# Kernel tuning notes

Hardware: AMD Instinct MI355X
Metric: run time of the kernel (lower is better)

## Reference

```python
import jax, jax.numpy as jnp
import numpy as np
from jax import lax


def setup_inputs() -> dict:
    key = jax.random.key(0)
    k1, k2 = jax.random.split(key)
    N, D_IN, D_MODEL, ORDER_K = 8192, 1024, 1024, 8
    scale = 1.0 / np.sqrt(D_IN)
    x = jax.random.normal(k1, (N, D_IN), dtype=jnp.float32)
    weights = jax.random.normal(k2, (ORDER_K + 1, D_IN, D_MODEL), dtype=jnp.float32) * scale
    return {"x": x, "weights": weights}


def reference(x, weights):
    # x: [N, d_in]; weights: [K+1, d_in, d_model]
    x32 = x.astype(jnp.float32)
    t0 = jnp.ones_like(x32)                      # T_0(x) = 1
    out = t0 @ weights[0] + x32 @ weights[1]     # T_0 W_0 + T_1 W_1

    def step(carry, w_k):
        prev2, prev1, acc = carry
        tk = 2.0 * x32 * prev1 - prev2           # Chebyshev recurrence T_k
        acc = acc + tk @ w_k
        return (prev1, tk, acc), None

    (_, _, out), _ = lax.scan(step, (t0, x32, out), weights[2:])
    return out
```

## Files before the change

kernel.cpp:

```cpp
#include <hip/hip_runtime.h>
#include <hip/hip_bf16.h>
#include <stdint.h>

typedef float  f32x4  __attribute__((ext_vector_type(4)));
typedef short  s16x8  __attribute__((ext_vector_type(8)));

#define GLOAD_LDS16(g, l)                                                          \
  __builtin_amdgcn_global_load_lds(                                               \
      (const __attribute__((address_space(1))) unsigned int*)(g),                 \
      (__attribute__((address_space(3))) unsigned int*)(l), 16, 0, 0)

#define WAITVM_(N) asm volatile("s_waitcnt vmcnt(" #N ")" ::: "memory")
#define WAITVM(N) WAITVM_(N)
#define WAITLGKM0 asm volatile("s_waitcnt lgkmcnt(0)" ::: "memory")

static __device__ __forceinline__ unsigned short f2bf(float f) {
  union { __hip_bfloat16 b; unsigned short s; } cv;
  cv.b = __float2bfloat16(f);
  return cv.s;
}

static __device__ __forceinline__ int swz_e(int r) { return ((r & 3) ^ ((r >> 2) & 1)); }
static __device__ __forceinline__ int swz_byte(int r, int c) {
  return r * 64 + (((c ^ swz_e(r)) & 3) << 4);
}

__global__ __launch_bounds__(256) void agen(const float* __restrict__ x,
                                            short* __restrict__ amat) {
  const int g = blockIdx.x * 256 + threadIdx.x;
  const int row = g >> 7;
  const int d0 = (g & 127) << 3;
  const float* xp = x + (size_t)row * 1024 + d0;
  f32x4 a = *(const f32x4*)xp, b = *(const f32x4*)(xp + 4);
  float p1[8], p2[8], x2[8];
  #pragma unroll
  for (int i = 0; i < 8; ++i) {
    float v = (i < 4) ? a[i] : b[i - 4];
    p1[i] = v; p2[i] = 1.f; x2[i] = v + v;
  }
  short* dst = amat + (size_t)row * 8192 + d0;
  #pragma unroll
  for (int k = 1; k <= 8; ++k) {
    union { unsigned short u[8]; s16x8 v; } o;
    #pragma unroll
    for (int i = 0; i < 8; ++i) o.u[i] = f2bf(p1[i]);
    *(s16x8*)(dst + (size_t)(k - 1) * 1024) = o.v;
    if (k < 8) {
      #pragma unroll
      for (int i = 0; i < 8; ++i) {
        float c = fmaf(x2[i], p1[i], -p2[i]);
        p2[i] = p1[i]; p1[i] = c;
      }
    }
  }
}

__global__ __launch_bounds__(256) void transpose_w2(const float* __restrict__ w,
                                                    short* __restrict__ wt) {
  __shared__ unsigned int ldsT[64 * 33];
  const int t = threadIdx.x;
  const int bid = blockIdx.x;
  const int kk = bid >> 8;
  const int db = (bid >> 4) & 15;
  const int cb = bid & 15;
  const int d0 = db * 64, c0 = cb * 64;
  const float* src = w + (size_t)(kk + 1) * 1048576 + (size_t)d0 * 1024 + c0;
  #pragma unroll
  for (int p = 0; p < 4; ++p) {
    int dl = p * 16 + (t >> 4);
    int c4 = (t & 15) * 4;
    f32x4 f = *(const f32x4*)(src + (size_t)dl * 1024 + c4);
    unsigned lo = (unsigned)f2bf(f.x) | ((unsigned)f2bf(f.y) << 16);
    unsigned hi = (unsigned)f2bf(f.z) | ((unsigned)f2bf(f.w) << 16);
    ldsT[dl * 33 + (t & 15) * 2]     = lo;
    ldsT[dl * 33 + (t & 15) * 2 + 1] = hi;
  }
  __syncthreads();
  const int col = t >> 2;
  const int dc  = t & 3;
  union { unsigned short u[8]; s16x8 v; } o0, o1;
  #pragma unroll
  for (int j = 0; j < 16; ++j) {
    int dl = dc * 16 + j;
    unsigned word = ldsT[dl * 33 + (col >> 1)];
    unsigned short e = (col & 1) ? (unsigned short)(word >> 16) : (unsigned short)(word & 0xffffu);
    if (j < 8) o0.u[j] = e; else o1.u[j - 8] = e;
  }
  short* dst = wt + (size_t)(c0 + col) * 8192 + (size_t)kk * 1024 + d0 + dc * 16;
  *(s16x8*)dst       = o0.v;
  *(s16x8*)(dst + 8) = o1.v;
}

__global__ __launch_bounds__(256) void transpose_w(const float* __restrict__ w,
                                                   short* __restrict__ wt) {
  __shared__ unsigned int ldsT[64 * 33];
  const int t = threadIdx.x;
  const int bid = blockIdx.x;
  const int kb = bid >> 8;
  const int db = (bid >> 4) & 15;
  const int cb = bid & 15;
  const int d0 = db * 64, c0 = cb * 64;
  const float* src = w + (size_t)(kb + 1) * 1048576 + (size_t)d0 * 1024 + c0;
  #pragma unroll
  for (int p = 0; p < 4; ++p) {
    int dl = p * 16 + (t >> 4);
    int c4 = (t & 15) * 4;
    f32x4 f = *(const f32x4*)(src + (size_t)dl * 1024 + c4);
    unsigned lo = (unsigned)f2bf(f.x) | ((unsigned)f2bf(f.y) << 16);
    unsigned hi = (unsigned)f2bf(f.z) | ((unsigned)f2bf(f.w) << 16);
    ldsT[dl * 33 + (t & 15) * 2]     = lo;
    ldsT[dl * 33 + (t & 15) * 2 + 1] = hi;
  }
  __syncthreads();
  const int col = t >> 2;
  const int dc  = t & 3;
  union { unsigned short u[8]; s16x8 v; } o0, o1;
  #pragma unroll
  for (int j = 0; j < 16; ++j) {
    int dl = dc * 16 + j;
    unsigned word = ldsT[dl * 33 + (col >> 1)];
    unsigned short e = (col & 1) ? (unsigned short)(word >> 16) : (unsigned short)(word & 0xffffu);
    if (j < 8) o0.u[j] = e; else o1.u[j - 8] = e;
  }
  short* dst = wt + ((size_t)(kb * 1024 + c0 + col) * 1024 + d0 + dc * 16);
  *(s16x8*)dst       = o0.v;
  *(s16x8*)(dst + 8) = o1.v;
}

__global__ __launch_bounds__(256) void bias_k(const float* __restrict__ w,
                                              float* __restrict__ b) {
  __shared__ float red[256];
  const int t = threadIdx.x;
  const int col = blockIdx.x * 64 + (t & 63);
  const int seg = t >> 6;
  float s = 0.f;
  const float* p = w + (size_t)(seg * 256) * 1024 + col;
  for (int d = 0; d < 256; ++d) s += p[(size_t)d * 1024];
  red[t] = s;
  __syncthreads();
  if (t < 64) b[col] = red[t] + red[t + 64] + red[t + 128] + red[t + 192];
}

__global__ __launch_bounds__(256) void init_out(const float* __restrict__ bias,
                                                float* __restrict__ out, int has_bias) {
  const size_t i = (size_t)blockIdx.x * 256 + threadIdx.x;
  const int c = (int)((i * 4) & 1023);
  f32x4 v = has_bias ? *(const f32x4*)(bias + c) : (f32x4){0.f, 0.f, 0.f, 0.f};
  *(f32x4*)(out + i * 4) = v;
}

__global__ __launch_bounds__(512, 2) void gemm8(
    const short* __restrict__ amat, const short* __restrict__ wt2,
    float* __restrict__ out) {
  __shared__ __attribute__((aligned(16))) char lds[131072];

  const int tid = threadIdx.x, lane = tid & 63, wid = tid >> 6;
  const int bid = blockIdx.x;
  const int xcd = bid & 7, mb = bid >> 3;
  const int nb = xcd >> 1, kb = xcd & 1;
  const int rowbase = mb * 256, colbase = nb * 256;
  const int wr = wid >> 2, wc = wid & 3;
  const int la = lane & 15, lg = lane >> 4;
  const int ela = (la & 3) ^ ((la >> 2) & 1);

  int aoff[4], boff[4];
  #pragma unroll
  for (int mm = 0; mm < 4; ++mm)
    aoff[mm] = ((wr * 128 + mm * 16 + la) << 6) + ((lg ^ ela) << 4);
  #pragma unroll
  for (int n = 0; n < 4; ++n)
    boff[n] = 65536 + ((wc * 64 + n * 16 + la) << 6) + ((lg ^ ela) << 4);

  const int rr   = lane >> 2;
  const int goff = ((lane & 3) ^ ((rr & 3) ^ ((rr >> 2) & 1))) * 8;
  const int r0 = wid * 32 + rr, r1 = r0 + 16;
  const size_t kk0 = (size_t)kb * 4096;
  const short* asrc0 = amat + (size_t)(rowbase + r0) * 8192 + kk0 + goff;
  const short* asrc1 = amat + (size_t)(rowbase + r1) * 8192 + kk0 + goff;
  const short* bsrc0 = wt2 + (size_t)(colbase + r0) * 8192 + kk0 + goff;
  const short* bsrc1 = wt2 + (size_t)(colbase + r1) * 8192 + kk0 + goff;
  const int adst0 = wid * 2048, adst1 = adst0 + 1024;

  f32x4 acc[8][4];
  #pragma unroll
  for (int m = 0; m < 8; ++m)
    #pragma unroll
    for (int n = 0; n < 4; ++n) acc[m][n] = (f32x4){0.f, 0.f, 0.f, 0.f};

#define STAGE_A(T, SOFF)                                                           \
  { GLOAD_LDS16(asrc0 + (T) * 32, lds + (SOFF) + adst0);                           \
    GLOAD_LDS16(asrc1 + (T) * 32, lds + (SOFF) + adst1); }
#define STAGE_B(T, SOFF)                                                           \
  { GLOAD_LDS16(bsrc0 + (T) * 32, lds + 65536 + (SOFF) + adst0);                   \
    GLOAD_LDS16(bsrc1 + (T) * 32, lds + 65536 + (SOFF) + adst1); }

  STAGE_A(0, 0);     STAGE_B(0, 0);
  STAGE_A(1, 16384); STAGE_B(1, 16384);
  WAITVM(4);
  __builtin_amdgcn_sched_barrier(0);
  __builtin_amdgcn_s_barrier();
  __builtin_amdgcn_sched_barrier(0);

  #pragma unroll 1
  for (int t = 0; t < 128; ++t) {
    const int soff = (t & 3) << 14;
    const int s2   = ((t + 2) & 3) << 14;
    s16x8 bf[4], af[4];

    #pragma unroll
    for (int n = 0; n < 4; ++n) bf[n] = *(const s16x8*)(lds + soff + boff[n]);
    #pragma unroll
    for (int mm = 0; mm < 4; ++mm) af[mm] = *(const s16x8*)(lds + soff + aoff[mm]);
    if (t + 2 < 128) STAGE_A(t + 2, s2);
    __builtin_amdgcn_s_barrier();
    WAITLGKM0;
    __builtin_amdgcn_sched_barrier(0);
    __builtin_amdgcn_s_setprio(1);
    #pragma unroll
    for (int n = 0; n < 4; ++n)
      #pragma unroll
      for (int mm = 0; mm < 4; ++mm)
        acc[mm][n] = __builtin_amdgcn_mfma_f32_16x16x32_bf16(af[mm], bf[n], acc[mm][n], 0, 0, 0);
    __builtin_amdgcn_s_setprio(0);
    __builtin_amdgcn_sched_barrier(0);
    __builtin_amdgcn_s_barrier();
    __builtin_amdgcn_sched_barrier(0);

    #pragma unroll
    for (int mm = 0; mm < 4; ++mm) af[mm] = *(const s16x8*)(lds + soff + 4096 + aoff[mm]);
    if (t + 2 < 128) STAGE_B(t + 2, s2);
    __builtin_amdgcn_s_barrier();
    WAITLGKM0;
    __builtin_amdgcn_sched_barrier(0);
    __builtin_amdgcn_s_setprio(1);
    #pragma unroll
    for (int n = 0; n < 4; ++n)
      #pragma unroll
      for (int mm = 0; mm < 4; ++mm)
        acc[4 + mm][n] = __builtin_amdgcn_mfma_f32_16x16x32_bf16(af[mm], bf[n], acc[4 + mm][n], 0, 0, 0);
    __builtin_amdgcn_s_setprio(0);
    if (t < 126) { WAITVM(4); } else { WAITVM(0); }
    __builtin_amdgcn_sched_barrier(0);
    __builtin_amdgcn_s_barrier();
    __builtin_amdgcn_sched_barrier(0);
  }
#undef STAGE_A
#undef STAGE_B

  #pragma unroll
  for (int m = 0; m < 8; ++m) {
    const int r0o = rowbase + wr * 128 + m * 16 + lg * 4;
    #pragma unroll
    for (int n = 0; n < 4; ++n) {
      const int c = colbase + wc * 64 + n * 16 + la;
      #pragma unroll
      for (int j = 0; j < 4; ++j)
        unsafeAtomicAdd(&out[(size_t)(r0o + j) * 1024 + c], acc[m][n][j]);
    }
  }
}

template <bool USE_WS>
__global__ __launch_bounds__(256, 2) void cheb_gemm(
    const float* __restrict__ x, const float* __restrict__ w,
    const short* __restrict__ wt, float* __restrict__ out) {
  __shared__ short Asm[2][4096];
  __shared__ short Bsm[3][8192];

  const int tid = threadIdx.x, lane = tid & 63, wid = tid >> 6;
  const int bid = blockIdx.x;
  const int xcd = bid & 7;
  const int mb  = bid >> 3;
  const int nb  = xcd >> 1, kb = xcd & 1;
  const int rowbase = mb * 128, colbase = nb * 256;
  const int kbase = kb * 512;
  const int wr = wid >> 1, wc = wid & 1;
  const int la = lane & 15, lg = lane >> 4;
  const int e_la = (la & 3) ^ ((la >> 2) & 1);
  const int abase = (wr * 64 + la) * 64 + ((lg ^ e_la) << 4);
  const int bbase = (wc * 128 + la) * 64 + ((lg ^ e_la) << 4);

  const int arow = tid & 127, h = tid >> 7;
  const int aw0 = swz_byte(arow, 2 * h), aw1 = swz_byte(arow, 2 * h + 1);
  const float* xrow = x + (size_t)(rowbase + arow) * 1024 + kbase + h * 16;

  float p1[16], p2[16];
  unsigned x2h[8];
  f32x4 xq[4];
  f32x4 acc[4][8];
  #pragma unroll
  for (int m = 0; m < 4; ++m)
    #pragma unroll
    for (int n = 0; n < 8; ++n) acc[m][n] = (f32x4){0.f, 0.f, 0.f, 0.f};

  if constexpr (USE_WS) {
    const int bcol0  = wid * 64 + (lane >> 2);
    const int goff   = ((lane & 3) ^ swz_e(lane >> 2)) * 8;
    const short* gptr = wt + (size_t)(colbase + bcol0) * 1024 + kbase + goff;

#define ISSUE_AT(PTR, WOFF)                                                        \
    { _Pragma("unroll")                                                            \
      for (int j_ = 0; j_ < 4; ++j_)                                               \
        GLOAD_LDS16((PTR) + j_ * 16384,                                            \
                    (char*)&Bsm[0][0] + (WOFF) + (wid * 4 + j_) * 1024); }

    #pragma unroll
    for (int q = 0; q < 4; ++q) xq[q] = *(const f32x4*)(xrow + q * 4);
    ISSUE_AT(gptr, 0);          gptr += 1048576;
    ISSUE_AT(gptr, 16384);      gptr += 1048576;
    {
      union { unsigned short u[8]; s16x8 v; } o0, o1;
      #pragma unroll
      for (int i = 0; i < 16; ++i) { p1[i] = xq[i >> 2][i & 3]; p2[i] = 1.f; }
      #pragma unroll
      for (int i = 0; i < 8; ++i) {
        union { unsigned u; _Float16 f[2]; } t2;
        t2.f[0] = (_Float16)(p1[2 * i] + p1[2 * i]);
        t2.f[1] = (_Float16)(p1[2 * i + 1] + p1[2 * i + 1]);
        x2h[i] = t2.u;
        o0.u[i] = f2bf(p1[i]); o1.u[i] = f2bf(p1[i + 8]);
      }
      *(s16x8*)((char*)&Asm[0][0] + aw0) = o0.v;
      *(s16x8*)((char*)&Asm[0][0] + aw1) = o1.v;
    }
    WAITLGKM0;
    WAITVM(4);
    __builtin_amdgcn_sched_barrier(0);
    __builtin_amdgcn_s_barrier();
    __builtin_amdgcn_sched_barrier(0);

    int wroff = 32768, rdoff = 0, ard = 0;

    #pragma unroll 1
    for (int t = 0; t < 128; ++t) {
      if ((t & 7) == 2 && t < 120) {
        const float* xs = xrow + ((t >> 3) + 1) * 32;
        #pragma unroll
        for (int q = 0; q < 4; ++q) xq[q] = *(const f32x4*)(xs + q * 4);
      }
      if (t + 2 < 128) {
        ISSUE_AT(gptr, wroff);
        gptr += ((t & 7) == 5) ? (32 - 7 * 1048576) : 1048576;
        wroff = (wroff == 32768) ? 0 : wroff + 16384;
      }
      if (t + 1 < 128) {
        const int rn = (t + 1) & 7;
        union { unsigned short u[8]; s16x8 v; } o0, o1;
        if (rn == 0) {
          #pragma unroll
          for (int i = 0; i < 16; ++i) { p1[i] = xq[i >> 2][i & 3]; p2[i] = 1.f; }
          #pragma unroll
          for (int i = 0; i < 8; ++i) {
            union { unsigned u; _Float16 f[2]; } t2;
            t2.f[0] = (_Float16)(p1[2 * i] + p1[2 * i]);
            t2.f[1] = (_Float16)(p1[2 * i + 1] + p1[2 * i + 1]);
            x2h[i] = t2.u;
            o0.u[i] = f2bf(p1[i]); o1.u[i] = f2bf(p1[i + 8]);
          }
        } else {
          #pragma unroll
          for (int i = 0; i < 16; ++i) {
            union { unsigned u; _Float16 f[2]; } t2; t2.u = x2h[i >> 1];
            float cur = fmaf((float)t2.f[i & 1], p1[i], -p2[i]);
            p2[i] = p1[i]; p1[i] = cur;
            unsigned short e = f2bf(cur);
            if (i < 8) o0.u[i] = e; else o1.u[i - 8] = e;
          }
        }
        *(s16x8*)((char*)&Asm[0][0] + (ard ^ 8192) + aw0) = o0.v;
        *(s16x8*)((char*)&Asm[0][0] + (ard ^ 8192) + aw1) = o1.v;
      }
      s16x8 af[4];
      #pragma unroll
      for (int m = 0; m < 4; ++m)
        af[m] = *(const s16x8*)((char*)&Asm[0][0] + ard + abase + m * 1024);
      #pragma unroll
      for (int n = 0; n < 8; ++n) {
        s16x8 bfr = *(const s16x8*)((char*)&Bsm[0][0] + rdoff + bbase + n * 1024);
        #pragma unroll
        for (int m = 0; m < 4; ++m)
          acc[m][n] = __builtin_amdgcn_mfma_f32_16x16x32_bf16(af[m], bfr, acc[m][n], 0, 0, 0);
      }
      WAITLGKM0;
      if (t < 126) { WAITVM(4); } else { WAITVM(0); }
      __builtin_amdgcn_sched_barrier(0);
      __builtin_amdgcn_s_barrier();
      __builtin_amdgcn_sched_barrier(0);
      rdoff = (rdoff == 32768) ? 0 : rdoff + 16384;
      ard ^= 8192;
    }
#undef ISSUE_AT
  } else {
    #pragma unroll 1
    for (int s = 0; s < 144; ++s) {
      const int r = s % 9, st = s / 9;
      const int d0 = kbase + st * 32;
      __syncthreads();
      { const int dd = tid & 31, cg = tid >> 5;
        const float* ws_ = w + (size_t)r * 1048576 + (size_t)(d0 + dd) * 1024 + colbase + cg * 4;
        #pragma unroll
        for (int p_ = 0; p_ < 8; ++p_) {
          f32x4 f_ = *(const f32x4*)(ws_ + p_ * 32);
          #pragma unroll
          for (int jj = 0; jj < 4; ++jj) {
            int col = cg * 4 + p_ * 32 + jj;
            int byt = col * 64 + ((dd & 7) << 1) + ((((dd >> 3) ^ swz_e(col)) & 3) << 4);
            *(unsigned short*)((char*)&Bsm[0][0] + byt) = f2bf(f_[jj]);
          } } }
      union { unsigned short u[8]; s16x8 v; } o0, o1;
      if (r == 0) {
        #pragma unroll
        for (int q = 0; q < 4; ++q) xq[q] = *(const f32x4*)(xrow + st * 32 + q * 4);
        #pragma unroll
        for (int i = 0; i < 16; ++i) { p1[i] = xq[i >> 2][i & 3]; p2[i] = 1.f; }
        #pragma unroll
        for (int i = 0; i < 8; ++i) {
          union { unsigned u; _Float16 f[2]; } t2;
          t2.f[0] = (_Float16)(p1[2 * i] + p1[2 * i]);
          t2.f[1] = (_Float16)(p1[2 * i + 1] + p1[2 * i + 1]);
          x2h[i] = t2.u;
          o0.u[i] = 0x3f80; o1.u[i] = 0x3f80;
        }
      } else if (r == 1) {
        #pragma unroll
        for (int i = 0; i < 8; ++i) { o0.u[i] = f2bf(p1[i]); o1.u[i] = f2bf(p1[i + 8]); }
      } else {
        #pragma unroll
        for (int i = 0; i < 16; ++i) {
          union { unsigned u; _Float16 f[2]; } t2; t2.u = x2h[i >> 1];
          float cur = fmaf((float)t2.f[i & 1], p1[i], -p2[i]);
          p2[i] = p1[i]; p1[i] = cur;
          if (i < 8) o0.u[i] = f2bf(cur); else o1.u[i - 8] = f2bf(cur);
        }
      }
      *(s16x8*)((char*)&Asm[0][0] + aw0) = o0.v;
      *(s16x8*)((char*)&Asm[0][0] + aw1) = o1.v;
      __syncthreads();
      s16x8 af[4];
      #pragma unroll
      for (int m = 0; m < 4; ++m)
        af[m] = *(const s16x8*)((char*)&Asm[0][0] + abase + m * 1024);
      #pragma unroll
      for (int n = 0; n < 8; ++n) {
        s16x8 bfr = *(const s16x8*)((char*)&Bsm[0][0] + bbase + n * 1024);
        #pragma unroll
        for (int m = 0; m < 4; ++m)
          acc[m][n] = __builtin_amdgcn_mfma_f32_16x16x32_bf16(af[m], bfr, acc[m][n], 0, 0, 0);
      }
    }
  }

  #pragma unroll
  for (int m = 0; m < 4; ++m) {
    const int r0 = rowbase + wr * 64 + m * 16 + lg * 4;
    #pragma unroll
    for (int n = 0; n < 8; ++n) {
      const int c = colbase + wc * 128 + n * 16 + la;
      #pragma unroll
      for (int j = 0; j < 4; ++j)
        unsafeAtomicAdd(&out[(size_t)(r0 + j) * 1024 + c], acc[m][n][j]);
    }
  }
}

extern "C" void kernel_launch(void* const* d_in, const int* in_sizes, int n_in,
                              void* d_out, int out_size, void* d_ws, size_t ws_size,
                              hipStream_t stream) {
  const float* x = (const float*)d_in[0];
  const float* w = (const float*)d_in[1];
  float* out = (float*)d_out;

  const size_t AMAT_BYTES = (size_t)8192 * 8192 * 2;
  const size_t WT2_BYTES  = (size_t)1024 * 8192 * 2;
  const size_t WT_BYTES   = (size_t)8 * 1024 * 1024 * 2;

  if (ws_size >= AMAT_BYTES + WT2_BYTES + 4096) {
    short* amat = (short*)d_ws;
    short* wt2  = (short*)((char*)d_ws + AMAT_BYTES);
    float* bias = (float*)((char*)d_ws + AMAT_BYTES + WT2_BYTES);
    agen<<<4096, 256, 0, stream>>>(x, amat);
    transpose_w2<<<2048, 256, 0, stream>>>(w, wt2);
    bias_k<<<16, 256, 0, stream>>>(w, bias);
    init_out<<<8192, 256, 0, stream>>>(bias, out, 1);
    gemm8<<<256, 512, 0, stream>>>(amat, wt2, out);
  } else if (ws_size >= WT_BYTES + 4096) {
    short* wt   = (short*)d_ws;
    float* bias = (float*)((char*)d_ws + WT_BYTES);
    transpose_w<<<2048, 256, 0, stream>>>(w, wt);
    bias_k<<<16, 256, 0, stream>>>(w, bias);
    init_out<<<8192, 256, 0, stream>>>(bias, out, 1);
    cheb_gemm<true><<<512, 256, 0, stream>>>(x, w, wt, out);
  } else {
    init_out<<<8192, 256, 0, stream>>>(nullptr, out, 0);
    cheb_gemm<false><<<512, 256, 0, stream>>>(x, w, nullptr, out);
  }
}
```

Measured before the change: 250.6 us.

## Retile GEMM to 64x1024 blocks with 4-way split-K and double buffering

Replaces the 256x256-tile, 2-way split-K GEMM with a kernel where each block computes a 64-row by full 1024-column output strip over one quarter of K, and each wave owns 128 columns. It launches 512 blocks instead of 256 and uses a two-stage LDS double buffer (139 KB) in place of the four-stage ring. The aim is more blocks for better CU coverage and reuse of the A tile across all columns. In exchange, B traffic per block rises, pipelining becomes shallower with a full vmcnt(0) wait each iteration, LDS use exceeds 128 KB so only one block fits per CU, and split-K atomics double.

```diff
diff --git a/kernel.cpp b/kernel.cpp
--- a/kernel.cpp
+++ b/kernel.cpp
@@ -149,69 +149,67 @@
   *(f32x4*)(out + i * 4) = v;
 }
 
-__global__ __launch_bounds__(512, 2) void gemm8(
+__global__ __launch_bounds__(512, 2) void gemm9(
     const short* __restrict__ amat, const short* __restrict__ wt2,
     float* __restrict__ out) {
-  __shared__ __attribute__((aligned(16))) char lds[131072];
+  __shared__ __attribute__((aligned(16))) char lds[139264];
 
   const int tid = threadIdx.x, lane = tid & 63, wid = tid >> 6;
   const int bid = blockIdx.x;
-  const int xcd = bid & 7, mb = bid >> 3;
-  const int nb = xcd >> 1, kb = xcd & 1;
-  const int rowbase = mb * 256, colbase = nb * 256;
-  const int wr = wid >> 2, wc = wid & 3;
+  const int xcd = bid & 7;
+  const int dq  = xcd >> 1;
+  const int mb  = ((bid >> 3) << 1) | (xcd & 1);
+  const int rowbase = mb * 64;
+  const size_t kq = (size_t)dq * 2048;
   const int la = lane & 15, lg = lane >> 4;
   const int ela = (la & 3) ^ ((la >> 2) & 1);
 
-  int aoff[4], boff[4];
-  #pragma unroll
-  for (int mm = 0; mm < 4; ++mm)
-    aoff[mm] = ((wr * 128 + mm * 16 + la) << 6) + ((lg ^ ela) << 4);
-  #pragma unroll
-  for (int n = 0; n < 4; ++n)
-    boff[n] = 65536 + ((wc * 64 + n * 16 + la) << 6) + ((lg ^ ela) << 4);
+  int aoff[4], boff[8];
+  #pragma unroll
+  for (int m = 0; m < 4; ++m)
+    aoff[m] = ((m * 16 + la) << 6) + ((lg ^ ela) << 4);
+  #pragma unroll
+  for (int n = 0; n < 8; ++n)
+    boff[n] = 8192 + ((wid * 128 + n * 16 + la) << 6) + ((lg ^ ela) << 4);
 
   const int rr   = lane >> 2;
-  const int goff = ((lane & 3) ^ ((rr & 3) ^ ((rr >> 2) & 1))) * 8;
-  const int r0 = wid * 32 + rr, r1 = r0 + 16;
-  const size_t kk0 = (size_t)kb * 4096;
-  const short* asrc0 = amat + (size_t)(rowbase + r0) * 8192 + kk0 + goff;
-  const short* asrc1 = amat + (size_t)(rowbase + r1) * 8192 + kk0 + goff;
-  const short* bsrc0 = wt2 + (size_t)(colbase + r0) * 8192 + kk0 + goff;
-  const short* bsrc1 = wt2 + (size_t)(colbase + r1) * 8192 + kk0 + goff;
-  const int adst0 = wid * 2048, adst1 = adst0 + 1024;
-
-  f32x4 acc[8][4];
-  #pragma unroll
-  for (int m = 0; m < 8; ++m)
-    #pragma unroll
-    for (int n = 0; n < 4; ++n) acc[m][n] = (f32x4){0.f, 0.f, 0.f, 0.f};
-
-#define STAGE_A(T, SOFF)                                                           \
-  { GLOAD_LDS16(asrc0 + (T) * 32, lds + (SOFF) + adst0);                           \
-    GLOAD_LDS16(asrc1 + (T) * 32, lds + (SOFF) + adst1); }
-#define STAGE_B(T, SOFF)                                                           \
-  { GLOAD_LDS16(bsrc0 + (T) * 32, lds + 65536 + (SOFF) + adst0);                   \
-    GLOAD_LDS16(bsrc1 + (T) * 32, lds + 65536 + (SOFF) + adst1); }
-
-  STAGE_A(0, 0);     STAGE_B(0, 0);
-  STAGE_A(1, 16384); STAGE_B(1, 16384);
-  WAITVM(4);
+  const int gchk = ((lane & 3) ^ ((rr & 3) ^ ((rr >> 2) & 1))) * 8;
+  const short* asrc = amat + (size_t)(rowbase + wid * 16 + rr) * 8192 + kq + gchk;
+  const short* bsrc = wt2 + (size_t)(wid * 128 + rr) * 8192 + kq + gchk;
+  const int bstep = 16 * 8192;
+
+  f32x4 acc[4][8];
+  #pragma unroll
+  for (int m = 0; m < 4; ++m)
+    #pragma unroll
+    for (int n = 0; n < 8; ++n) acc[m][n] = (f32x4){0.f, 0.f, 0.f, 0.f};
+
+#define STAGE_A(T, PAR)                                                            \
+  { if (wid < 4) GLOAD_LDS16(asrc + (T) * 32, lds + (PAR) * 4096 + wid * 1024); }
+#define STAGE_B(T, PAR, J0, J1)                                                    \
+  { _Pragma("unroll")                                                              \
+    for (int j_ = (J0); j_ < (J1); ++j_)                                           \
+      GLOAD_LDS16(bsrc + (size_t)j_ * bstep + (T) * 32,                            \
+                  lds + 8192 + (PAR) * 65536 + (wid * 8 + j_) * 1024); }
+
+  STAGE_A(0, 0);
+  STAGE_B(0, 0, 0, 8);
+  WAITVM(0);
   __builtin_amdgcn_sched_barrier(0);
   __builtin_amdgcn_s_barrier();
   __builtin_amdgcn_sched_barrier(0);
 
   #pragma unroll 1
-  for (int t = 0; t < 128; ++t) {
-    const int soff = (t & 3) << 14;
-    const int s2   = ((t + 2) & 3) << 14;
-    s16x8 bf[4], af[4];
-
-    #pragma unroll
-    for (int n = 0; n < 4; ++n) bf[n] = *(const s16x8*)(lds + soff + boff[n]);
-    #pragma unroll
-    for (int mm = 0; mm < 4; ++mm) af[mm] = *(const s16x8*)(lds + soff + aoff[mm]);
-    if (t + 2 < 128) STAGE_A(t + 2, s2);
+  for (int t = 0; t < 64; ++t) {
+    const int par = t & 1;
+    const int ao = par * 4096, bo = par * 65536;
+    s16x8 af[4], bf[4];
+
+    #pragma unroll
+    for (int m = 0; m < 4; ++m) af[m] = *(const s16x8*)(lds + ao + aoff[m]);
+    #pragma unroll
+    for (int n = 0; n < 4; ++n) bf[n] = *(const s16x8*)(lds + bo + boff[n]);
+    if (t < 63) { STAGE_A(t + 1, par ^ 1); STAGE_B(t + 1, par ^ 1, 0, 4); }
     __builtin_amdgcn_s_barrier();
     WAITLGKM0;
     __builtin_amdgcn_sched_barrier(0);
@@ -219,16 +217,16 @@
     #pragma unroll
     for (int n = 0; n < 4; ++n)
       #pragma unroll
-      for (int mm = 0; mm < 4; ++mm)
-        acc[mm][n] = __builtin_amdgcn_mfma_f32_16x16x32_bf16(af[mm], bf[n], acc[mm][n], 0, 0, 0);
+      for (int m = 0; m < 4; ++m)
+        acc[m][n] = __builtin_amdgcn_mfma_f32_16x16x32_bf16(af[m], bf[n], acc[m][n], 0, 0, 0);
     __builtin_amdgcn_s_setprio(0);
     __builtin_amdgcn_sched_barrier(0);
     __builtin_amdgcn_s_barrier();
     __builtin_amdgcn_sched_barrier(0);
 
     #pragma unroll
-    for (int mm = 0; mm < 4; ++mm) af[mm] = *(const s16x8*)(lds + soff + 4096 + aoff[mm]);
-    if (t + 2 < 128) STAGE_B(t + 2, s2);
+    for (int n = 0; n < 4; ++n) bf[n] = *(const s16x8*)(lds + bo + boff[4 + n]);
+    if (t < 63) STAGE_B(t + 1, par ^ 1, 4, 8);
     __builtin_amdgcn_s_barrier();
     WAITLGKM0;
     __builtin_amdgcn_sched_barrier(0);
@@ -236,10 +234,10 @@
     #pragma unroll
     for (int n = 0; n < 4; ++n)
       #pragma unroll
-      for (int mm = 0; mm < 4; ++mm)
-        acc[4 + mm][n] = __builtin_amdgcn_mfma_f32_16x16x32_bf16(af[mm], bf[n], acc[4 + mm][n], 0, 0, 0);
+      for (int m = 0; m < 4; ++m)
+        acc[m][4 + n] = __builtin_amdgcn_mfma_f32_16x16x32_bf16(af[m], bf[n], acc[m][4 + n], 0, 0, 0);
     __builtin_amdgcn_s_setprio(0);
-    if (t < 126) { WAITVM(4); } else { WAITVM(0); }
+    if (t < 63) { WAITVM(0); }
     __builtin_amdgcn_sched_barrier(0);
     __builtin_amdgcn_s_barrier();
     __builtin_amdgcn_sched_barrier(0);
@@ -248,14 +246,14 @@
 #undef STAGE_B
 
   #pragma unroll
-  for (int m = 0; m < 8; ++m) {
-    const int r0o = rowbase + wr * 128 + m * 16 + lg * 4;
-    #pragma unroll
-    for (int n = 0; n < 4; ++n) {
-      const int c = colbase + wc * 64 + n * 16 + la;
+  for (int m = 0; m < 4; ++m) {
+    const int r0 = rowbase + m * 16 + lg * 4;
+    #pragma unroll
+    for (int n = 0; n < 8; ++n) {
+      const int c = wid * 128 + n * 16 + la;
       #pragma unroll
       for (int j = 0; j < 4; ++j)
-        unsafeAtomicAdd(&out[(size_t)(r0o + j) * 1024 + c], acc[m][n][j]);
+        unsafeAtomicAdd(&out[(size_t)(r0 + j) * 1024 + c], acc[m][n][j]);
     }
   }
 }
@@ -482,7 +480,7 @@
     transpose_w2<<<2048, 256, 0, stream>>>(w, wt2);
     bias_k<<<16, 256, 0, stream>>>(w, bias);
     init_out<<<8192, 256, 0, stream>>>(bias, out, 1);
-    gemm8<<<256, 512, 0, stream>>>(amat, wt2, out);
+    gemm9<<<512, 512, 0, stream>>>(amat, wt2, out);
   } else if (ws_size >= WT_BYTES + 4096) {
     short* wt   = (short*)d_ws;
     float* bias = (float*)((char*)d_ws + WT_BYTES);
```

New measurement: 344.9 us. 1.38x slower.

## Shrink GEMM LDS staging to triple-buffered A and double-buffered B

Applied to the files above, without the earlier changes.

Restructures the bf16 MFMA GEMM's LDS pipeline from four shared stages of A and B (128 KB) to three A buffers and two B buffers (80 KB). B for the next step is prefetched one iteration ahead and A two ahead, with adjusted vmcnt waits. This cuts LDS footprint, which could allow more resident blocks per CU. In exchange it shortens B's prefetch distance, which may expose global load latency.

```diff
diff --git a/kernel.cpp b/kernel.cpp
--- a/kernel.cpp
+++ b/kernel.cpp
@@ -149,37 +149,35 @@
   *(f32x4*)(out + i * 4) = v;
 }
 
-__global__ __launch_bounds__(512, 2) void gemm8(
+__global__ __launch_bounds__(512, 2) void gemm10(
     const short* __restrict__ amat, const short* __restrict__ wt2,
     float* __restrict__ out) {
-  __shared__ __attribute__((aligned(16))) char lds[131072];
+  __shared__ __attribute__((aligned(16))) char lds[81920];
 
   const int tid = threadIdx.x, lane = tid & 63, wid = tid >> 6;
   const int bid = blockIdx.x;
-  const int xcd = bid & 7, mb = bid >> 3;
+  const int xcd = bid & 7;
   const int nb = xcd >> 1, kb = xcd & 1;
+  const int mb = bid >> 3;
   const int rowbase = mb * 256, colbase = nb * 256;
+  const size_t kq = (size_t)kb * 4096;
   const int wr = wid >> 2, wc = wid & 3;
   const int la = lane & 15, lg = lane >> 4;
   const int ela = (la & 3) ^ ((la >> 2) & 1);
 
-  int aoff[4], boff[4];
-  #pragma unroll
-  for (int mm = 0; mm < 4; ++mm)
-    aoff[mm] = ((wr * 128 + mm * 16 + la) << 6) + ((lg ^ ela) << 4);
+  int aoff[8], boff[4];
+  #pragma unroll
+  for (int m = 0; m < 8; ++m)
+    aoff[m] = ((wr * 128 + m * 16 + la) << 6) + ((lg ^ ela) << 4);
   #pragma unroll
   for (int n = 0; n < 4; ++n)
-    boff[n] = 65536 + ((wc * 64 + n * 16 + la) << 6) + ((lg ^ ela) << 4);
+    boff[n] = ((wc * 64 + n * 16 + la) << 6) + ((lg ^ ela) << 4);
 
   const int rr   = lane >> 2;
-  const int goff = ((lane & 3) ^ ((rr & 3) ^ ((rr >> 2) & 1))) * 8;
-  const int r0 = wid * 32 + rr, r1 = r0 + 16;
-  const size_t kk0 = (size_t)kb * 4096;
-  const short* asrc0 = amat + (size_t)(rowbase + r0) * 8192 + kk0 + goff;
-  const short* asrc1 = amat + (size_t)(rowbase + r1) * 8192 + kk0 + goff;
-  const short* bsrc0 = wt2 + (size_t)(colbase + r0) * 8192 + kk0 + goff;
-  const short* bsrc1 = wt2 + (size_t)(colbase + r1) * 8192 + kk0 + goff;
-  const int adst0 = wid * 2048, adst1 = adst0 + 1024;
+  const int gchk = ((lane & 3) ^ ((rr & 3) ^ ((rr >> 2) & 1))) * 8;
+  const short* asrc = amat + (size_t)(rowbase + wid * 32 + rr) * 8192 + kq + gchk;
+  const short* bsrc = wt2 + (size_t)(colbase + wid * 32 + rr) * 8192 + kq + gchk;
+  const int sdst = wid * 2048 + (lane & 3) * 0;
 
   f32x4 acc[8][4];
   #pragma unroll
@@ -187,31 +185,35 @@
     #pragma unroll
     for (int n = 0; n < 4; ++n) acc[m][n] = (f32x4){0.f, 0.f, 0.f, 0.f};
 
-#define STAGE_A(T, SOFF)                                                           \
-  { GLOAD_LDS16(asrc0 + (T) * 32, lds + (SOFF) + adst0);                           \
-    GLOAD_LDS16(asrc1 + (T) * 32, lds + (SOFF) + adst1); }
-#define STAGE_B(T, SOFF)                                                           \
-  { GLOAD_LDS16(bsrc0 + (T) * 32, lds + 65536 + (SOFF) + adst0);                   \
-    GLOAD_LDS16(bsrc1 + (T) * 32, lds + 65536 + (SOFF) + adst1); }
-
-  STAGE_A(0, 0);     STAGE_B(0, 0);
-  STAGE_A(1, 16384); STAGE_B(1, 16384);
-  WAITVM(4);
+#define STAGE_A(T, BUF)                                                            \
+  { GLOAD_LDS16(asrc + (size_t)(T) * 32,              lds + (BUF) * 16384 + wid * 2048);        \
+    GLOAD_LDS16(asrc + 16 * 8192 + (size_t)(T) * 32,  lds + (BUF) * 16384 + wid * 2048 + 1024); }
+#define STAGE_B(T, BUF)                                                            \
+  { GLOAD_LDS16(bsrc + (size_t)(T) * 32,              lds + 49152 + (BUF) * 16384 + wid * 2048);        \
+    GLOAD_LDS16(bsrc + 16 * 8192 + (size_t)(T) * 32,  lds + 49152 + (BUF) * 16384 + wid * 2048 + 1024); }
+
+  STAGE_A(0, 0);
+  STAGE_B(0, 0);
+  STAGE_A(1, 1);
+  WAITVM(2);
   __builtin_amdgcn_sched_barrier(0);
   __builtin_amdgcn_s_barrier();
   __builtin_amdgcn_sched_barrier(0);
 
+  int ar = 0;
+  int aw = 2;
+
   #pragma unroll 1
   for (int t = 0; t < 128; ++t) {
-    const int soff = (t & 3) << 14;
-    const int s2   = ((t + 2) & 3) << 14;
+    const int ao = ar * 16384;
+    const int bo = 49152 + (t & 1) * 16384;
     s16x8 bf[4], af[4];
 
     #pragma unroll
-    for (int n = 0; n < 4; ++n) bf[n] = *(const s16x8*)(lds + soff + boff[n]);
-    #pragma unroll
-    for (int mm = 0; mm < 4; ++mm) af[mm] = *(const s16x8*)(lds + soff + aoff[mm]);
-    if (t + 2 < 128) STAGE_A(t + 2, s2);
+    for (int n = 0; n < 4; ++n) bf[n] = *(const s16x8*)(lds + bo + boff[n]);
+    #pragma unroll
+    for (int m = 0; m < 4; ++m) af[m] = *(const s16x8*)(lds + ao + aoff[m]);
+    if (t < 127) STAGE_B(t + 1, (t + 1) & 1);
     __builtin_amdgcn_s_barrier();
     WAITLGKM0;
     __builtin_amdgcn_sched_barrier(0);
@@ -219,16 +221,16 @@
     #pragma unroll
     for (int n = 0; n < 4; ++n)
       #pragma unroll
-      for (int mm = 0; mm < 4; ++mm)
-        acc[mm][n] = __builtin_amdgcn_mfma_f32_16x16x32_bf16(af[mm], bf[n], acc[mm][n], 0, 0, 0);
+      for (int m = 0; m < 4; ++m)
+        acc[m][n] = __builtin_amdgcn_mfma_f32_16x16x32_bf16(af[m], bf[n], acc[m][n], 0, 0, 0);
     __builtin_amdgcn_s_setprio(0);
     __builtin_amdgcn_sched_barrier(0);
     __builtin_amdgcn_s_barrier();
     __builtin_amdgcn_sched_barrier(0);
 
     #pragma unroll
-    for (int mm = 0; mm < 4; ++mm) af[mm] = *(const s16x8*)(lds + soff + 4096 + aoff[mm]);
-    if (t + 2 < 128) STAGE_B(t + 2, s2);
+    for (int m = 0; m < 4; ++m) af[m] = *(const s16x8*)(lds + ao + aoff[4 + m]);
+    if (t < 126) STAGE_A(t + 2, aw);
     __builtin_amdgcn_s_barrier();
     WAITLGKM0;
     __builtin_amdgcn_sched_barrier(0);
@@ -236,26 +238,29 @@
     #pragma unroll
     for (int n = 0; n < 4; ++n)
       #pragma unroll
-      for (int mm = 0; mm < 4; ++mm)
-        acc[4 + mm][n] = __builtin_amdgcn_mfma_f32_16x16x32_bf16(af[mm], bf[n], acc[4 + mm][n], 0, 0, 0);
+      for (int m = 0; m < 4; ++m)
+        acc[4 + m][n] = __builtin_amdgcn_mfma_f32_16x16x32_bf16(af[m], bf[n], acc[4 + m][n], 0, 0, 0);
     __builtin_amdgcn_s_setprio(0);
-    if (t < 126) { WAITVM(4); } else { WAITVM(0); }
+    if (t < 126) { WAITVM(2); } else { WAITVM(0); }
     __builtin_amdgcn_sched_barrier(0);
     __builtin_amdgcn_s_barrier();
     __builtin_amdgcn_sched_barrier(0);
+
+    ar = (ar == 2) ? 0 : ar + 1;
+    aw = (aw == 2) ? 0 : aw + 1;
   }
 #undef STAGE_A
 #undef STAGE_B
 
   #pragma unroll
   for (int m = 0; m < 8; ++m) {
-    const int r0o = rowbase + wr * 128 + m * 16 + lg * 4;
+    const int r0 = rowbase + wr * 128 + m * 16 + lg * 4;
     #pragma unroll
     for (int n = 0; n < 4; ++n) {
       const int c = colbase + wc * 64 + n * 16 + la;
       #pragma unroll
       for (int j = 0; j < 4; ++j)
-        unsafeAtomicAdd(&out[(size_t)(r0o + j) * 1024 + c], acc[m][n][j]);
+        unsafeAtomicAdd(&out[(size_t)(r0 + j) * 1024 + c], acc[m][n][j]);
     }
   }
 }
@@ -482,7 +487,7 @@
     transpose_w2<<<2048, 256, 0, stream>>>(w, wt2);
     bias_k<<<16, 256, 0, stream>>>(w, bias);
     init_out<<<8192, 256, 0, stream>>>(bias, out, 1);
-    gemm8<<<256, 512, 0, stream>>>(amat, wt2, out);
+    gemm10<<<256, 512, 0, stream>>>(amat, wt2, out);
   } else if (ws_size >= WT_BYTES + 4096) {
     short* wt   = (short*)d_ws;
     float* bias = (float*)((char*)d_ws + WT_BYTES);
```

Measured after the change: 249.3 us. About the same (-0.5%).
